# Performance work log

Hardware: AMD Instinct MI355X
Metric: run time of the kernel (lower is better)

The kernel has to match this reference:

```python
import jax, jax.numpy as jnp
import numpy as np

B, NIN, NREG, D, H, L = 8, 1024, 16, 1024, 16, 12
DFF = 4 * D
S = NIN + NREG
HD = D // H
EPS = 1e-6


def setup_inputs() -> dict:
    key = jax.random.key(0)
    ks = jax.random.split(key, 8)
    p = lambda k, shape: jax.random.normal(k, shape, jnp.float32) * 0.02
    return dict(
        x=jax.random.normal(ks[0], (B, S, D), jnp.float32),
        n_input=NIN,
        ln1_g=jnp.ones((L, D), jnp.float32), ln1_b=jnp.zeros((L, D), jnp.float32),
        wqkv=p(ks[1], (L, D, 3 * D)), bqkv=jnp.zeros((L, 3 * D), jnp.float32),
        wo=p(ks[2], (L, D, D)), bo=jnp.zeros((L, D), jnp.float32),
        ln2_g=jnp.ones((L, D), jnp.float32), ln2_b=jnp.zeros((L, D), jnp.float32),
        w1=p(ks[3], (L, D, DFF)), b1=jnp.zeros((L, DFF), jnp.float32),
        w2=p(ks[4], (L, DFF, D)), b2=jnp.zeros((L, D), jnp.float32),
        lnf_g=jnp.ones((D,), jnp.float32), lnf_b=jnp.zeros((D,), jnp.float32),
    )


def _ln(x, g, b):
    mu = x.mean(-1, keepdims=True)
    var = ((x - mu) ** 2).mean(-1, keepdims=True)
    return (x - mu) * jax.lax.rsqrt(var + EPS) * g + b


def _build_mask(n_input, total):
    # inputs attend everywhere; registers attend to all inputs and causally among registers
    i = jnp.arange(total)[:, None]
    j = jnp.arange(total)[None, :]
    blocked = (i >= n_input) & (j >= n_input) & (j > i)
    return jnp.where(blocked, -jnp.inf, 0.0).astype(jnp.float32)  # (S, S) additive


def _attn(h, wqkv_l, bqkv_l, wo_l, bo_l, mask):
    b, s, _ = h.shape
    qkv = h @ wqkv_l + bqkv_l                                   # (B,S,3D)
    q, k, v = jnp.split(qkv, 3, axis=-1)
    q = q.reshape(b, s, H, HD).transpose(0, 2, 1, 3)            # (B,H,S,HD)
    k = k.reshape(b, s, H, HD).transpose(0, 2, 1, 3)
    v = v.reshape(b, s, H, HD).transpose(0, 2, 1, 3)
    scores = jnp.einsum('bhqd,bhkd->bhqk', q, k) / np.sqrt(HD) + mask
    a = jax.nn.softmax(scores, axis=-1)
    o = jnp.einsum('bhqk,bhkd->bhqd', a, v)
    o = o.transpose(0, 2, 1, 3).reshape(b, s, D)
    return o @ wo_l + bo_l


def reference(x, n_input, ln1_g, ln1_b, wqkv, bqkv, wo, bo,
              ln2_g, ln2_b, w1, b1, w2, b2, lnf_g, lnf_b):
    mask = _build_mask(n_input, x.shape[1])

    def blk(h, p):
        l1g, l1b, wq, bq, wo_, bo_, l2g, l2b, w1_, b1_, w2_, b2_ = p
        h = h + _attn(_ln(h, l1g, l1b), wq, bq, wo_, bo_, mask)
        u = _ln(h, l2g, l2b) @ w1_ + b1_
        h = h + jax.nn.gelu(u) @ w2_ + b2_
        return h, None

    h, _ = jax.lax.scan(blk, x, (ln1_g, ln1_b, wqkv, bqkv, wo, bo,
                                 ln2_g, ln2_b, w1, b1, w2, b2))
    return _ln(h, lnf_g, lnf_b)
```

## Files before the change

### kernel.cpp

```cpp
#include <hip/hip_runtime.h>
#include <hip/hip_bf16.h>
#include <stdint.h>

#define DD   1024
#define TD   3072
#define DFFN 4096
#define NL   12
#define SS   1040
#define SP   1056
#define BB   8
#define MM   (BB*SS)
#define HH   16
#define NTAIL 16

typedef float  f32x4  __attribute__((ext_vector_type(4)));
typedef __bf16 bf16x8 __attribute__((ext_vector_type(8)));
typedef unsigned short u16;

union Bf8 { bf16x8 v; u16 s[8]; };

__device__ __forceinline__ u16 f2b(float f) {
  union { float f; unsigned u; } x; x.f = f;
  unsigned r = (x.u + 0x7FFFu + ((x.u >> 16) & 1u)) >> 16;
  return (u16)r;
}

__device__ __forceinline__ f32x4 mfma_bf16(bf16x8 a, bf16x8 b, f32x4 c) {
  return __builtin_amdgcn_mfma_f32_16x16x32_bf16(a, b, c, 0, 0, 0);
}

__device__ __forceinline__ void gload_lds16(const u16* g, u16* l) {
  __builtin_amdgcn_global_load_lds((const __attribute__((address_space(1))) void*)g,
                                   (__attribute__((address_space(3))) void*)l, 16, 0, 0);
}

__device__ __forceinline__ float dppmax16(float t) {
  union { float f; int i; } u, v;
  u.f = t;
  v.i = __builtin_amdgcn_update_dpp(0, u.i, 0xB1, 0xF, 0xF, true);
  u.f = fmaxf(u.f, v.f);
  v.i = __builtin_amdgcn_update_dpp(0, u.i, 0x4E, 0xF, 0xF, true);
  u.f = fmaxf(u.f, v.f);
  v.i = __builtin_amdgcn_update_dpp(0, u.i, 0x124, 0xF, 0xF, true);
  u.f = fmaxf(u.f, v.f);
  v.i = __builtin_amdgcn_update_dpp(0, u.i, 0x128, 0xF, 0xF, true);
  u.f = fmaxf(u.f, v.f);
  return u.f;
}

__global__ __launch_bounds__(256)
void transpose_cast(const float* __restrict__ in, u16* __restrict__ out, int K, int N) {
  __shared__ float tile[32][33];
  const int n0 = blockIdx.x * 32, k0 = blockIdx.y * 32;
  const size_t lb = (size_t)blockIdx.z * K * N;
  const int tx = threadIdx.x, ty = threadIdx.y;
  for (int j = 0; j < 4; ++j)
    tile[ty + 8*j][tx] = in[lb + (size_t)(k0 + ty + 8*j) * N + n0 + tx];
  __syncthreads();
  for (int j = 0; j < 4; ++j)
    out[lb + (size_t)(n0 + ty + 8*j) * K + k0 + tx] = f2b(tile[tx][ty + 8*j]);
}

template<int OUTF>
__global__ __launch_bounds__(256)
void ln_kernel(const float* __restrict__ in, const float* __restrict__ gam,
               const float* __restrict__ bet, u16* __restrict__ outb, float* __restrict__ outf) {
  const int row = blockIdx.x, t = threadIdx.x;
  const float4 v = ((const float4*)(in + (size_t)row * DD))[t];
  float s  = v.x + v.y + v.z + v.w;
  float s2 = v.x*v.x + v.y*v.y + v.z*v.z + v.w*v.w;
  for (int off = 1; off < 64; off <<= 1) { s += __shfl_xor(s, off); s2 += __shfl_xor(s2, off); }
  __shared__ float red[8];
  if ((t & 63) == 0) { red[t >> 6] = s; red[4 + (t >> 6)] = s2; }
  __syncthreads();
  s  = red[0] + red[1] + red[2] + red[3];
  s2 = red[4] + red[5] + red[6] + red[7];
  const float mu = s * (1.0f/1024.0f);
  const float var = s2 * (1.0f/1024.0f) - mu*mu;
  const float rs = rsqrtf(var + 1e-6f);
  const float4 gv = ((const float4*)gam)[t];
  const float4 bv = ((const float4*)bet)[t];
  const float y0 = (v.x - mu)*rs*gv.x + bv.x;
  const float y1 = (v.y - mu)*rs*gv.y + bv.y;
  const float y2 = (v.z - mu)*rs*gv.z + bv.z;
  const float y3 = (v.w - mu)*rs*gv.w + bv.w;
  if (OUTF) {
    float4 o; o.x=y0; o.y=y1; o.z=y2; o.w=y3;
    ((float4*)(outf + (size_t)row * DD))[t] = o;
  } else {
    ushort4 o; o.x=f2b(y0); o.y=f2b(y1); o.z=f2b(y2); o.w=f2b(y3);
    ((ushort4*)(outb + (size_t)row * DD))[t] = o;
  }
}

template<int EPI>
__global__ __launch_bounds__(256, 2)
void gemm_bt(const u16* __restrict__ A, const u16* __restrict__ Bt,
             const float* __restrict__ bias, const float* __restrict__ resid,
             float* outF, u16* outB,
             u16* __restrict__ qb, u16* __restrict__ kb, u16* __restrict__ vtb,
             int N, int K) {
  __shared__ u16 As[128*64];
  __shared__ u16 Bs[128*64];
  const int tid = threadIdx.x;

  const int nwg = gridDim.x * gridDim.y;
  int wgid = blockIdx.y * gridDim.x + blockIdx.x;
  wgid = (wgid & 7) * (nwg >> 3) + (wgid >> 3);
  const int mb = wgid % gridDim.x;
  const int nb = wgid / gridDim.x;
  const int m0 = mb * 128, n0 = nb * 128;

  const int lane = tid & 63, w = tid >> 6;
  const int wr = (w >> 1) * 64, wc = (w & 1) * 64;
  const int c = lane & 15, g = lane >> 4;

  f32x4 acc[4][4];
  for (int i = 0; i < 4; ++i) for (int j = 0; j < 4; ++j) acc[i][j] = f32x4{0.f,0.f,0.f,0.f};

  const int srow = tid >> 3, scg = tid & 7;
  const size_t aoff = (size_t)(m0 + srow) * K + scg * 8;
  const size_t boff = (size_t)(n0 + srow) * K + scg * 8;

  for (int kt = 0; kt < K; kt += 64) {
    for (int it = 0; it < 4; ++it) {
      gload_lds16(A  + aoff + (size_t)it * 32 * K + kt, As + (it*256 + tid) * 8);
      gload_lds16(Bt + boff + (size_t)it * 32 * K + kt, Bs + (it*256 + tid) * 8);
    }
    __syncthreads();
    for (int kk = 0; kk < 2; ++kk) {
      bf16x8 af[4], bfr[4];
      for (int i = 0; i < 4; ++i) af[i]  = *(const bf16x8*)(As + (wr + i*16 + c)*64 + kk*32 + g*8);
      for (int j = 0; j < 4; ++j) bfr[j] = *(const bf16x8*)(Bs + (wc + j*16 + c)*64 + kk*32 + g*8);
      for (int i = 0; i < 4; ++i)
        for (int j = 0; j < 4; ++j)
          acc[i][j] = mfma_bf16(af[i], bfr[j], acc[i][j]);
    }
    __syncthreads();
  }

  for (int j = 0; j < 4; ++j) {
    const int col = n0 + wc + j*16 + c;
    const float bcol = bias[col];
    for (int i = 0; i < 4; ++i) {
      const int row0 = m0 + wr + i*16 + 4*g;
      if (EPI == 3) {
        const int part = col >> 10;
        const int hh2  = (col >> 6) & 15;
        const int hd   = col & 63;
        const int bb   = (int)((unsigned)row0 / SS);
        const int s0   = row0 - bb * SS;
        const size_t bh = (size_t)(bb * HH + hh2);
        if (part == 2) {
          ushort4 pk;
          pk.x = f2b(acc[i][j][0] + bcol);
          pk.y = f2b(acc[i][j][1] + bcol);
          pk.z = f2b(acc[i][j][2] + bcol);
          pk.w = f2b(acc[i][j][3] + bcol);
          *(ushort4*)(vtb + (bh*64 + hd)*SP + s0) = pk;
        } else if (part == 0) {
          for (int r = 0; r < 4; ++r)
            qb[(bh*SP + s0 + r)*64 + hd] = f2b((acc[i][j][r] + bcol) * 0.125f);
        } else {
          for (int r = 0; r < 4; ++r)
            kb[(bh*SP + s0 + r)*64 + hd] = f2b(acc[i][j][r] + bcol);
        }
      } else {
        for (int r = 0; r < 4; ++r) {
          const size_t idx = (size_t)(row0 + r) * N + col;
          const float v = acc[i][j][r] + bcol;
          if (EPI == 0) {
            outF[idx] = v;
          } else if (EPI == 1) {
            const float z = 1.5957691216f * (v + 0.044715f * v * v * v);
            const float e = __expf(z);
            outB[idx] = f2b(v * e * __builtin_amdgcn_rcpf(e + 1.0f));
          } else {
            outF[idx] = v + resid[idx];
          }
        }
      }
    }
  }
}

__global__ __launch_bounds__(512, 8)
void attn_staged(const u16* __restrict__ Qb, const u16* __restrict__ Kb,
                 const u16* __restrict__ VTb, u16* __restrict__ out,
                 const int* __restrict__ npt) {
  __shared__ u16 KV[2][4096];
  __shared__ u16 PT[8][640];
  const int tid = threadIdx.x;
  const int w = tid >> 6, lane = tid & 63;
  const int c = lane & 15, g = lane >> 4;
  const int nin = npt[0];
  u16* pw = PT[w];

  if (blockIdx.x < NTAIL) {
    const int bh = blockIdx.x * 8 + w;
    const int b = bh >> 4, hh = bh & 15;
    const int q0 = 64 * 16;

    bf16x8 aq0, aq1;
    {
      const u16* qp = Qb + ((size_t)bh * SP + q0 + c) * 64 + g * 8;
      aq0 = *(const bf16x8*)qp;
      aq1 = *(const bf16x8*)(qp + 32);
    }

    float m[4], ls[4];
    f32x4 o[4];
    int qrow[4];
    for (int r = 0; r < 4; ++r) { m[r] = -1e30f; ls[r] = 0.f; qrow[r] = q0 + 4*g + r; }
    for (int nd = 0; nd < 4; ++nd) o[nd] = f32x4{0.f,0.f,0.f,0.f};

    for (int kt = 0; kt < 33; ++kt) {
      const int k0 = kt * 32;

      f32x4 s[2];
      {
        const u16* kp0 = Kb + ((size_t)bh * SP + k0 + c) * 64 + g * 8;
        f32x4 z0 = f32x4{0.f,0.f,0.f,0.f};
        z0 = mfma_bf16(aq0, *(const bf16x8*)kp0, z0);
        z0 = mfma_bf16(aq1, *(const bf16x8*)(kp0 + 32), z0);
        s[0] = z0;
        const u16* kp1 = kp0 + 16 * 64;
        f32x4 z1 = f32x4{0.f,0.f,0.f,0.f};
        z1 = mfma_bf16(aq0, *(const bf16x8*)kp1, z1);
        z1 = mfma_bf16(aq1, *(const bf16x8*)(kp1 + 32), z1);
        s[1] = z1;
      }

      for (int jt = 0; jt < 2; ++jt) {
        const int j = k0 + jt*16 + c;
        for (int r = 0; r < 4; ++r) {
          const int q = qrow[r];
          const bool blocked = (j >= SS) || ((q >= nin) && (j >= nin) && (j > q));
          if (blocked) s[jt][r] = -1e30f;
        }
      }

      for (int r = 0; r < 4; ++r) {
        float t = fmaxf(s[0][r], s[1][r]);
        for (int off = 1; off < 16; off <<= 1) t = fmaxf(t, __shfl_xor(t, off));
        const float mn = fmaxf(m[r], t);
        const float al = __expf(m[r] - mn);
        m[r] = mn;
        const float p0 = __expf(s[0][r] - mn);
        const float p1 = __expf(s[1][r] - mn);
        s[0][r] = p0; s[1][r] = p1;
        float ps = p0 + p1;
        for (int off = 1; off < 16; off <<= 1) ps += __shfl_xor(ps, off);
        ls[r] = ls[r] * al + ps;
        for (int nd = 0; nd < 4; ++nd) o[nd][r] *= al;
      }

      for (int jt = 0; jt < 2; ++jt)
        for (int r = 0; r < 4; ++r)
          pw[(4*g + r)*40 + jt*16 + c] = f2b(s[jt][r]);
      __builtin_amdgcn_sched_barrier(0);
      bf16x8 ap = *(const bf16x8*)(pw + c*40 + 8*g);
      __builtin_amdgcn_sched_barrier(0);

      for (int nd = 0; nd < 4; ++nd) {
        const u16* vp = VTb + ((size_t)bh * 64 + nd*16 + c) * SP + k0 + 8*g;
        o[nd] = mfma_bf16(ap, *(const bf16x8*)vp, o[nd]);
      }
    }

    for (int nd = 0; nd < 4; ++nd)
      for (int r = 0; r < 4; ++r) {
        const float v = o[nd][r] / ls[r];
        out[((size_t)b * SS + qrow[r]) * DD + hh*64 + nd*16 + c] = f2b(v);
      }
    return;
  }

  const int sb = blockIdx.x - NTAIL;
  const int bh = sb & 127;
  const int qt = (sb >> 7) * 8 + w;
  const int b = bh >> 4, hh = bh & 15;
  const int q0 = qt * 16;

  const u16* ssrc; int kstr; u16* sdst;
  if (tid < 256) {
    const int row = tid >> 3, col8 = (tid & 7) ^ (row & 7);
    ssrc = Kb + ((size_t)bh * SP + row) * 64 + col8 * 8;
    kstr = 32 * 64;
    sdst = &KV[0][tid * 8];
  } else {
    const int t2 = tid - 256, row = t2 >> 2, col8 = (t2 & 3) ^ (row & 3);
    ssrc = VTb + ((size_t)bh * 64 + row) * SP + col8 * 8;
    kstr = 32;
    sdst = &KV[0][2048 + t2 * 8];
  }
#define STAGE(bufbit, kt) gload_lds16(ssrc + (size_t)(kt) * kstr, sdst + (bufbit) * 4096)

  bf16x8 aq0, aq1;
  {
    const u16* qp = Qb + ((size_t)bh * SP + q0 + c) * 64 + g * 8;
    aq0 = *(const bf16x8*)qp;
    aq1 = *(const bf16x8*)(qp + 32);
  }

  Bf8 onesf;
  for (int i = 0; i < 8; ++i) onesf.s[i] = (c == 0) ? (u16)0x3F80 : (u16)0;

  float m[4];
  f32x4 o[5];
  int qrow[4];
  for (int r = 0; r < 4; ++r) { m[r] = -1e30f; qrow[r] = q0 + 4*g + r; }
  for (int nd = 0; nd < 5; ++nd) o[nd] = f32x4{0.f,0.f,0.f,0.f};

  const bool tile_regs = (q0 + 15) >= nin;
  const int c7 = c & 7, c3 = c & 3;

  STAGE(0, 0);

  for (int kt = 0; kt < 33; ++kt) {
    const int buf = kt & 1;
    __syncthreads();
    if (kt < 32) STAGE(buf ^ 1, kt + 1);
    const u16* Kt = &KV[buf][0];
    const u16* Vt = &KV[buf][2048];
    const int k0 = kt * 32;

    f32x4 s[2];
    {
      bf16x8 k00 = *(const bf16x8*)(Kt + c*64        + ((g    ) ^ c7) * 8);
      bf16x8 k01 = *(const bf16x8*)(Kt + c*64        + ((g + 4) ^ c7) * 8);
      f32x4 z0 = f32x4{0.f,0.f,0.f,0.f};
      z0 = mfma_bf16(aq0, k00, z0);
      z0 = mfma_bf16(aq1, k01, z0);
      s[0] = z0;
      bf16x8 k10 = *(const bf16x8*)(Kt + (c+16)*64   + ((g    ) ^ c7) * 8);
      bf16x8 k11 = *(const bf16x8*)(Kt + (c+16)*64   + ((g + 4) ^ c7) * 8);
      f32x4 z1 = f32x4{0.f,0.f,0.f,0.f};
      z1 = mfma_bf16(aq0, k10, z1);
      z1 = mfma_bf16(aq1, k11, z1);
      s[1] = z1;
    }

    if (tile_regs || (k0 + 31 >= SS)) {
      for (int jt = 0; jt < 2; ++jt) {
        const int j = k0 + jt*16 + c;
        for (int r = 0; r < 4; ++r) {
          const int q = qrow[r];
          const bool blocked = (j >= SS) || ((q >= nin) && (j >= nin) && (j > q));
          if (blocked) s[jt][r] = -1e30f;
        }
      }
    }

    for (int r = 0; r < 4; ++r) {
      const float t = dppmax16(fmaxf(s[0][r], s[1][r]));
      const float mn = fmaxf(m[r], t);
      const float al = __expf(m[r] - mn);
      m[r] = mn;
      for (int nd = 0; nd < 5; ++nd) o[nd][r] *= al;
      s[0][r] = __expf(s[0][r] - mn);
      s[1][r] = __expf(s[1][r] - mn);
    }

    for (int jt = 0; jt < 2; ++jt)
      for (int r = 0; r < 4; ++r)
        pw[(4*g + r)*40 + jt*16 + c] = f2b(s[jt][r]);
    __builtin_amdgcn_sched_barrier(0);
    bf16x8 ap = *(const bf16x8*)(pw + c*40 + 8*g);
    __builtin_amdgcn_sched_barrier(0);

    for (int nd = 0; nd < 4; ++nd) {
      bf16x8 bv = *(const bf16x8*)(Vt + (nd*16 + c)*32 + ((g ^ c3) * 8));
      o[nd] = mfma_bf16(ap, bv, o[nd]);
    }
    o[4] = mfma_bf16(ap, onesf.v, o[4]);
  }
#undef STAGE

  float rls[4];
  for (int r = 0; r < 4; ++r)
    rls[r] = 1.0f / __shfl(o[4][r], lane & 48);
  for (int nd = 0; nd < 4; ++nd)
    for (int r = 0; r < 4; ++r)
      out[((size_t)b * SS + qrow[r]) * DD + hh*64 + nd*16 + c] = f2b(o[nd][r] * rls[r]);
}

extern "C" void kernel_launch(void* const* d_in, const int* in_sizes, int n_in,
                              void* d_out, int out_size, void* d_ws, size_t ws_size,
                              hipStream_t stream) {
  const float* x    = (const float*)d_in[0];
  const int*   npt  = (const int*)  d_in[1];
  const float* ln1g = (const float*)d_in[2];
  const float* ln1b = (const float*)d_in[3];
  const float* wqkv = (const float*)d_in[4];
  const float* bqkv = (const float*)d_in[5];
  const float* wo   = (const float*)d_in[6];
  const float* bo   = (const float*)d_in[7];
  const float* ln2g = (const float*)d_in[8];
  const float* ln2b = (const float*)d_in[9];
  const float* w1   = (const float*)d_in[10];
  const float* b1   = (const float*)d_in[11];
  const float* w2   = (const float*)d_in[12];
  const float* b2   = (const float*)d_in[13];
  const float* lnfg = (const float*)d_in[14];
  const float* lnfb = (const float*)d_in[15];

  char* ws = (char*)d_ws;
  size_t off = 0;
  u16*   wqkvT = (u16*)(ws + off);   off += (size_t)NL*TD*DD*2;
  u16*   woT   = (u16*)(ws + off);   off += (size_t)NL*DD*DD*2;
  u16*   w1T   = (u16*)(ws + off);   off += (size_t)NL*DFFN*DD*2;
  u16*   w2T   = (u16*)(ws + off);   off += (size_t)NL*DD*DFFN*2;
  float* h     = (float*)(ws + off); off += (size_t)MM*DD*4;
  u16*   lnb   = (u16*)(ws + off);   off += (size_t)MM*DD*2;
  u16*   Qb    = (u16*)(ws + off);   off += (size_t)BB*HH*SP*64*2;
  u16*   Kb    = (u16*)(ws + off);   off += (size_t)BB*HH*SP*64*2;
  u16*   VTb   = (u16*)(ws + off);   off += (size_t)BB*HH*64*SP*2;
  u16*   attnO = (u16*)(ws + off);   off += (size_t)MM*DD*2;
  u16*   ffh   = (u16*)(ws + off);   off += (size_t)MM*DFFN*2;

  const dim3 tb(32, 8);
  transpose_cast<<<dim3(TD/32,   DD/32,   NL), tb, 0, stream>>>(wqkv, wqkvT, DD,   TD);
  transpose_cast<<<dim3(DD/32,   DD/32,   NL), tb, 0, stream>>>(wo,   woT,   DD,   DD);
  transpose_cast<<<dim3(DFFN/32, DD/32,   NL), tb, 0, stream>>>(w1,   w1T,   DD,   DFFN);
  transpose_cast<<<dim3(DD/32,   DFFN/32, NL), tb, 0, stream>>>(w2,   w2T,   DFFN, DD);
  hipMemcpyAsync(h, x, (size_t)MM*DD*4, hipMemcpyDeviceToDevice, stream);
  hipMemsetAsync(Qb, 0, (size_t)3*BB*HH*SP*64*2, stream);

  for (int l = 0; l < NL; ++l) {
    ln_kernel<0><<<MM, 256, 0, stream>>>(h, ln1g + (size_t)l*DD, ln1b + (size_t)l*DD, lnb, nullptr);
    gemm_bt<3><<<dim3(MM/128, TD/128), 256, 0, stream>>>(
        lnb, wqkvT + (size_t)l*TD*DD, bqkv + (size_t)l*TD, nullptr, nullptr, nullptr,
        Qb, Kb, VTb, TD, DD);
    attn_staged<<<dim3(BB*HH*8 + NTAIL), 512, 0, stream>>>(Qb, Kb, VTb, attnO, npt);
    gemm_bt<2><<<dim3(MM/128, DD/128), 256, 0, stream>>>(
        attnO, woT + (size_t)l*DD*DD, bo + (size_t)l*DD, h, h, nullptr,
        nullptr, nullptr, nullptr, DD, DD);
    ln_kernel<0><<<MM, 256, 0, stream>>>(h, ln2g + (size_t)l*DD, ln2b + (size_t)l*DD, lnb, nullptr);
    gemm_bt<1><<<dim3(MM/128, DFFN/128), 256, 0, stream>>>(
        lnb, w1T + (size_t)l*DFFN*DD, b1 + (size_t)l*DFFN, nullptr, nullptr, ffh,
        nullptr, nullptr, nullptr, DFFN, DD);
    gemm_bt<2><<<dim3(MM/128, DD/128), 256, 0, stream>>>(
        ffh, w2T + (size_t)l*DD*DFFN, b2 + (size_t)l*DD, h, h, nullptr,
        nullptr, nullptr, nullptr, DD, DFFN);
  }
  ln_kernel<1><<<MM, 256, 0, stream>>>(h, lnfg, lnfb, nullptr, (float*)d_out);
}
```

Baseline: 6.550 ms.

## Add 256x256 double-buffered swizzled GEMM for QKV and FFN-up projections

Adds a new 512-thread GEMM kernel with 256x256 tiles, double-buffered LDS staging through direct global-to-LDS loads, XOR-swizzled LDS layout, and interleaved MFMA/load scheduling with priority hints. It replaces the 128x128 GEMM for the QKV projection and the first FFN matmul. M is padded to 8448 so it tiles by 256, and the QKV epilogue skips the padded rows. The goal is more data reuse per tile and better overlap of memory and compute, at the cost of higher register and LDS pressure and extra work on the padded rows.

```diff
diff --git a/kernel.cpp b/kernel.cpp
--- a/kernel.cpp
+++ b/kernel.cpp
@@ -10,6 +10,7 @@
 #define SP   1056
 #define BB   8
 #define MM   (BB*SS)
+#define MP   8448
 #define HH   16
 #define NTAIL 16
 
@@ -97,9 +98,7 @@
 __global__ __launch_bounds__(256, 2)
 void gemm_bt(const u16* __restrict__ A, const u16* __restrict__ Bt,
              const float* __restrict__ bias, const float* __restrict__ resid,
-             float* outF, u16* outB,
-             u16* __restrict__ qb, u16* __restrict__ kb, u16* __restrict__ vtb,
-             int N, int K) {
+             float* outF, u16* outB, int N, int K) {
   __shared__ u16 As[128*64];
   __shared__ u16 Bs[128*64];
   const int tid = threadIdx.x;
@@ -144,40 +143,172 @@
     const float bcol = bias[col];
     for (int i = 0; i < 4; ++i) {
       const int row0 = m0 + wr + i*16 + 4*g;
+      for (int r = 0; r < 4; ++r) {
+        const size_t idx = (size_t)(row0 + r) * N + col;
+        const float v = acc[i][j][r] + bcol;
+        if (EPI == 1) {
+          const float z = 1.5957691216f * (v + 0.044715f * v * v * v);
+          const float e = __expf(z);
+          outB[idx] = f2b(v * e * __builtin_amdgcn_rcpf(e + 1.0f));
+        } else {
+          outF[idx] = v + resid[idx];
+        }
+      }
+    }
+  }
+}
+
+template<int EPI>
+__global__ __launch_bounds__(512, 2)
+void gemm256(const u16* __restrict__ A, const u16* __restrict__ Bt,
+             const float* __restrict__ bias, u16* __restrict__ outB,
+             u16* __restrict__ qb, u16* __restrict__ kb, u16* __restrict__ vtb,
+             int N, int K, int MT) {
+  __shared__ u16 As[2][256*64];
+  __shared__ u16 Bs[2][256*64];
+  const int tid = threadIdx.x;
+
+  const int nwg = gridDim.x;
+  const int q8 = nwg >> 3, r8 = nwg & 7;
+  const int xcd = blockIdx.x & 7, bidx = blockIdx.x >> 3;
+  const int wgid = (xcd < r8 ? xcd * (q8 + 1) : r8 * (q8 + 1) + (xcd - r8) * q8) + bidx;
+  const int mb = wgid % MT, nb = wgid / MT;
+  const int m0 = mb * 256, n0 = nb * 256;
+
+  const int lane = tid & 63, w = tid >> 6;
+  const int wr = w >> 2, wc = w & 3;
+  const int c = lane & 15, g = lane >> 4;
+  const int c7 = c & 7;
+
+  const int sr = tid >> 3;
+  const int s7 = tid & 7;
+  const int scg = s7 ^ (sr & 7);
+
+#define STG_A(bb, tt, hf) do { \
+    const int r0_ = (hf)*128 + sr, r1_ = r0_ + 64; \
+    gload_lds16(A + (size_t)(m0 + r0_) * K + (size_t)(tt)*64 + scg*8, &As[bb][r0_*64 + s7*8]); \
+    gload_lds16(A + (size_t)(m0 + r1_) * K + (size_t)(tt)*64 + scg*8, &As[bb][r1_*64 + s7*8]); \
+  } while (0)
+#define STG_B(bb, tt, hf) do { \
+    const int r0_ = (hf)*128 + sr, r1_ = r0_ + 64; \
+    gload_lds16(Bt + (size_t)(n0 + r0_) * K + (size_t)(tt)*64 + scg*8, &Bs[bb][r0_*64 + s7*8]); \
+    gload_lds16(Bt + (size_t)(n0 + r1_) * K + (size_t)(tt)*64 + scg*8, &Bs[bb][r1_*64 + s7*8]); \
+  } while (0)
+
+  f32x4 acc[8][4];
+#pragma unroll
+  for (int i = 0; i < 8; ++i)
+#pragma unroll
+    for (int j = 0; j < 4; ++j) acc[i][j] = f32x4{0.f,0.f,0.f,0.f};
+
+  bf16x8 breg[4][2], areg[2][2];
+
+#define RD_B(bb) do { _Pragma("unroll") \
+    for (int nf = 0; nf < 4; ++nf) { _Pragma("unroll") \
+      for (int kk = 0; kk < 2; ++kk) { \
+        const int row_ = wc*64 + nf*16 + c; \
+        const int grp_ = (kk*4 + g) ^ c7; \
+        breg[nf][kk] = *(const bf16x8*)(&Bs[bb][row_*64 + grp_*8]); } } } while (0)
+#define RD_A(bb, q) do { _Pragma("unroll") \
+    for (int mi = 0; mi < 2; ++mi) { _Pragma("unroll") \
+      for (int kk = 0; kk < 2; ++kk) { \
+        const int row_ = wr*128 + ((q)*2 + mi)*16 + c; \
+        const int grp_ = (kk*4 + g) ^ c7; \
+        areg[mi][kk] = *(const bf16x8*)(&As[bb][row_*64 + grp_*8]); } } } while (0)
+#define DO_MFMA(q) do { __builtin_amdgcn_s_setprio(1); _Pragma("unroll") \
+    for (int mi = 0; mi < 2; ++mi) { _Pragma("unroll") \
+      for (int nf = 0; nf < 4; ++nf) { _Pragma("unroll") \
+        for (int kk = 0; kk < 2; ++kk) \
+          acc[(q)*2 + mi][nf] = mfma_bf16(areg[mi][kk], breg[nf][kk], acc[(q)*2 + mi][nf]); } } \
+    __builtin_amdgcn_s_setprio(0); } while (0)
+#define SYNC1 do { __builtin_amdgcn_sched_barrier(0); __builtin_amdgcn_s_barrier(); \
+    asm volatile("s_waitcnt lgkmcnt(0)" ::: "memory"); \
+    __builtin_amdgcn_sched_barrier(0); } while (0)
+#define SYNC2 do { __builtin_amdgcn_sched_barrier(0); __builtin_amdgcn_s_barrier(); } while (0)
+
+  const int NT = K >> 6;
+  const int NIT = NT >> 1;
+
+  STG_B(0, 0, 0); STG_B(0, 0, 1);
+  STG_A(0, 0, 0); STG_A(0, 0, 1);
+  STG_B(1, 1, 0); STG_B(1, 1, 1);
+  __builtin_amdgcn_sched_barrier(0);
+  asm volatile("s_waitcnt vmcnt(4)" ::: "memory");
+  __builtin_amdgcn_s_barrier();
+
+  for (int it = 0; it < NIT; ++it) {
+    const int T0 = 2*it, T1 = T0 + 1;
+    const bool last = (it == NIT - 1);
+    RD_B(0); RD_A(0, 0); STG_A(1, T1, 0);
+    SYNC1; DO_MFMA(0); SYNC2;
+    RD_A(0, 1); STG_A(1, T1, 1);
+    SYNC1; DO_MFMA(1); SYNC2;
+    RD_A(0, 2); if (!last) STG_B(0, T0 + 2, 0);
+    SYNC1; DO_MFMA(2); SYNC2;
+    RD_A(0, 3); if (!last) STG_B(0, T0 + 2, 1);
+    SYNC1; DO_MFMA(3);
+    __builtin_amdgcn_sched_barrier(0);
+    if (last) asm volatile("s_waitcnt vmcnt(0)" ::: "memory");
+    else      asm volatile("s_waitcnt vmcnt(4)" ::: "memory");
+    __builtin_amdgcn_s_barrier();
+    RD_B(1); RD_A(1, 0); if (!last) STG_A(0, T0 + 2, 0);
+    SYNC1; DO_MFMA(0); SYNC2;
+    RD_A(1, 1); if (!last) STG_A(0, T0 + 2, 1);
+    SYNC1; DO_MFMA(1); SYNC2;
+    RD_A(1, 2); if (!last) STG_B(1, T1 + 2, 0);
+    SYNC1; DO_MFMA(2); SYNC2;
+    RD_A(1, 3); if (!last) STG_B(1, T1 + 2, 1);
+    SYNC1; DO_MFMA(3);
+    if (!last) {
+      __builtin_amdgcn_sched_barrier(0);
+      asm volatile("s_waitcnt vmcnt(4)" ::: "memory");
+      __builtin_amdgcn_s_barrier();
+    }
+  }
+#undef STG_A
+#undef STG_B
+#undef RD_B
+#undef RD_A
+#undef DO_MFMA
+#undef SYNC1
+#undef SYNC2
+
+#pragma unroll
+  for (int nf = 0; nf < 4; ++nf) {
+    const int col = n0 + wc*64 + nf*16 + c;
+    const float bcol = bias[col];
+#pragma unroll
+    for (int mf = 0; mf < 8; ++mf) {
+      const int row0 = m0 + wr*128 + mf*16 + 4*g;
       if (EPI == 3) {
-        const int part = col >> 10;
-        const int hh2  = (col >> 6) & 15;
-        const int hd   = col & 63;
-        const int bb   = (int)((unsigned)row0 / SS);
-        const int s0   = row0 - bb * SS;
-        const size_t bh = (size_t)(bb * HH + hh2);
-        if (part == 2) {
-          ushort4 pk;
-          pk.x = f2b(acc[i][j][0] + bcol);
-          pk.y = f2b(acc[i][j][1] + bcol);
-          pk.z = f2b(acc[i][j][2] + bcol);
-          pk.w = f2b(acc[i][j][3] + bcol);
-          *(ushort4*)(vtb + (bh*64 + hd)*SP + s0) = pk;
-        } else if (part == 0) {
-          for (int r = 0; r < 4; ++r)
-            qb[(bh*SP + s0 + r)*64 + hd] = f2b((acc[i][j][r] + bcol) * 0.125f);
-        } else {
-          for (int r = 0; r < 4; ++r)
-            kb[(bh*SP + s0 + r)*64 + hd] = f2b(acc[i][j][r] + bcol);
+        if (row0 < MM) {
+          const int part = col >> 10;
+          const int hh2  = (col >> 6) & 15;
+          const int hd   = col & 63;
+          const int bb   = (int)((unsigned)row0 / SS);
+          const int s0   = row0 - bb * SS;
+          const size_t bh = (size_t)(bb * HH + hh2);
+          if (part == 2) {
+            ushort4 pk;
+            pk.x = f2b(acc[mf][nf][0] + bcol);
+            pk.y = f2b(acc[mf][nf][1] + bcol);
+            pk.z = f2b(acc[mf][nf][2] + bcol);
+            pk.w = f2b(acc[mf][nf][3] + bcol);
+            *(ushort4*)(vtb + (bh*64 + hd)*SP + s0) = pk;
+          } else if (part == 0) {
+            for (int r = 0; r < 4; ++r)
+              qb[(bh*SP + s0 + r)*64 + hd] = f2b((acc[mf][nf][r] + bcol) * 0.125f);
+          } else {
+            for (int r = 0; r < 4; ++r)
+              kb[(bh*SP + s0 + r)*64 + hd] = f2b(acc[mf][nf][r] + bcol);
+          }
         }
       } else {
         for (int r = 0; r < 4; ++r) {
-          const size_t idx = (size_t)(row0 + r) * N + col;
-          const float v = acc[i][j][r] + bcol;
-          if (EPI == 0) {
-            outF[idx] = v;
-          } else if (EPI == 1) {
-            const float z = 1.5957691216f * (v + 0.044715f * v * v * v);
-            const float e = __expf(z);
-            outB[idx] = f2b(v * e * __builtin_amdgcn_rcpf(e + 1.0f));
-          } else {
-            outF[idx] = v + resid[idx];
-          }
+          const float v = acc[mf][nf][r] + bcol;
+          const float z = 1.5957691216f * (v + 0.044715f * v * v * v);
+          const float e = __expf(z);
+          outB[(size_t)(row0 + r) * N + col] = f2b(v * e * __builtin_amdgcn_rcpf(e + 1.0f));
         }
       }
     }
@@ -412,12 +543,12 @@
   u16*   w1T   = (u16*)(ws + off);   off += (size_t)NL*DFFN*DD*2;
   u16*   w2T   = (u16*)(ws + off);   off += (size_t)NL*DD*DFFN*2;
   float* h     = (float*)(ws + off); off += (size_t)MM*DD*4;
-  u16*   lnb   = (u16*)(ws + off);   off += (size_t)MM*DD*2;
+  u16*   lnb   = (u16*)(ws + off);   off += (size_t)MP*DD*2;
   u16*   Qb    = (u16*)(ws + off);   off += (size_t)BB*HH*SP*64*2;
   u16*   Kb    = (u16*)(ws + off);   off += (size_t)BB*HH*SP*64*2;
   u16*   VTb   = (u16*)(ws + off);   off += (size_t)BB*HH*64*SP*2;
   u16*   attnO = (u16*)(ws + off);   off += (size_t)MM*DD*2;
-  u16*   ffh   = (u16*)(ws + off);   off += (size_t)MM*DFFN*2;
+  u16*   ffh   = (u16*)(ws + off);   off += (size_t)MP*DFFN*2;
 
   const dim3 tb(32, 8);
   transpose_cast<<<dim3(TD/32,   DD/32,   NL), tb, 0, stream>>>(wqkv, wqkvT, DD,   TD);
@@ -429,20 +560,18 @@
 
   for (int l = 0; l < NL; ++l) {
     ln_kernel<0><<<MM, 256, 0, stream>>>(h, ln1g + (size_t)l*DD, ln1b + (size_t)l*DD, lnb, nullptr);
-    gemm_bt<3><<<dim3(MM/128, TD/128), 256, 0, stream>>>(
-        lnb, wqkvT + (size_t)l*TD*DD, bqkv + (size_t)l*TD, nullptr, nullptr, nullptr,
-        Qb, Kb, VTb, TD, DD);
+    gemm256<3><<<dim3((MP/256)*(TD/256)), 512, 0, stream>>>(
+        lnb, wqkvT + (size_t)l*TD*DD, bqkv + (size_t)l*TD, nullptr,
+        Qb, Kb, VTb, TD, DD, MP/256);
     attn_staged<<<dim3(BB*HH*8 + NTAIL), 512, 0, stream>>>(Qb, Kb, VTb, attnO, npt);
     gemm_bt<2><<<dim3(MM/128, DD/128), 256, 0, stream>>>(
-        attnO, woT + (size_t)l*DD*DD, bo + (size_t)l*DD, h, h, nullptr,
-        nullptr, nullptr, nullptr, DD, DD);
+        attnO, woT + (size_t)l*DD*DD, bo + (size_t)l*DD, h, h, nullptr, DD, DD);
     ln_kernel<0><<<MM, 256, 0, stream>>>(h, ln2g + (size_t)l*DD, ln2b + (size_t)l*DD, lnb, nullptr);
-    gemm_bt<1><<<dim3(MM/128, DFFN/128), 256, 0, stream>>>(
-        lnb, w1T + (size_t)l*DFFN*DD, b1 + (size_t)l*DFFN, nullptr, nullptr, ffh,
-        nullptr, nullptr, nullptr, DFFN, DD);
+    gemm256<1><<<dim3((MP/256)*(DFFN/256)), 512, 0, stream>>>(
+        lnb, w1T + (size_t)l*DFFN*DD, b1 + (size_t)l*DFFN, ffh,
+        nullptr, nullptr, nullptr, DFFN, DD, MP/256);
     gemm_bt<2><<<dim3(MM/128, DD/128), 256, 0, stream>>>(
-        ffh, w2T + (size_t)l*DD*DFFN, b2 + (size_t)l*DD, h, h, nullptr,
-        nullptr, nullptr, nullptr, DD, DFFN);
+        ffh, w2T + (size_t)l*DD*DFFN, b2 + (size_t)l*DD, h, h, nullptr, DD, DFFN);
   }
   ln_kernel<1><<<MM, 256, 0, stream>>>(h, lnfg, lnfb, nullptr, (float*)d_out);
 }
```

After: 6.941 ms. 1.06x slower.
